# Performance work log

Hardware: AMD Instinct MI355X
Metric: run time of the kernel (lower is better)

Reference implementation:

```python
import jax, jax.numpy as jnp
import numpy as np

DIST_EPS = 0.1   # distance_eps
NORM_EPS = 0.1   # norm_eps
QUAT_EPS = 1e-3
FA_EPS = 1e-5


def normed_vec(V):
    return V / jnp.sqrt((V ** 2).sum(-1, keepdims=True) + NORM_EPS)


def collect_neighbors(node_h, edge_idx):
    # node_h: (B,N,D), edge_idx: (B,N,K) -> (B,N,K,D)
    B, N, K = edge_idx.shape
    D = node_h.shape[-1]
    idx = jnp.broadcast_to(edge_idx.reshape(B, N * K, 1), (B, N * K, D))
    return jnp.take_along_axis(node_h, idx, axis=1).reshape(B, N, K, D)


def field_average(node_h, C, num_fields):
    # per-field mean, scattered back to residues; residues with C==0 get 0
    onehot = (C[..., None] == (jnp.arange(num_fields) + 1)).astype(node_h.dtype)  # (B,N,F)
    sums = jnp.einsum('bnf,bnd->bfd', onehot, node_h)
    counts = jnp.sum(onehot, axis=1)[..., None]  # (B,F,1)
    avg = sums / (counts + FA_EPS)
    return jnp.einsum('bnf,bfd->bnd', onehot, avg)


def reference_frames(X):
    X_N, X_CA, X_C = X[:, :, 0], X[:, :, 1], X[:, :, 2]
    u_CA_N = normed_vec(X_N - X_CA)
    u_CA_C = normed_vec(X_C - X_CA)
    n_1 = u_CA_N
    n_2 = normed_vec(jnp.cross(n_1, u_CA_C))
    n_3 = normed_vec(jnp.cross(n_1, n_2))
    return jnp.stack([n_1, n_2, n_3], -1)  # (B,N,3,3), frames as columns


def reference_frames_field(X, C, num_fields):
    X_N, X_CA, X_C = X[:, :, 0], X[:, :, 1], X[:, :, 2]
    u_CA_N_avg = field_average(normed_vec(X_N - X_CA), C, num_fields)
    u_CA_C_avg = field_average(normed_vec(X_C - X_CA), C, num_fields)
    n_1 = normed_vec(u_CA_N_avg)
    n_2 = normed_vec(jnp.cross(n_1, normed_vec(u_CA_C_avg)))
    n_3 = normed_vec(jnp.cross(n_1, n_2))
    return jnp.stack([n_1, n_2, n_3], -1)


def quaternions_from_rotations(R):
    Rf = R.reshape(R.shape[:-2] + (9,))
    R00, R01, R02, R10, R11, R12, R20, R21, R22 = [Rf[..., i] for i in range(9)]
    mag = 0.5 * jnp.sqrt(jnp.abs(1.0 + jnp.stack([
        R00 + R11 + R22,
        R00 - R11 - R22,
        -R00 + R11 - R22,
        -R00 - R11 + R22], -1)) + QUAT_EPS)
    signs = jnp.sign(jnp.stack([
        jnp.ones_like(R00), R21 - R12, R02 - R20, R10 - R01], -1))
    q = signs * mag
    return q / jnp.sqrt((q ** 2).sum(-1, keepdims=True))


def transformation_features(X_i, X_j, R_i, R_j):
    dX = X_j - X_i[:, :, None]                    # (B,N,K,3)
    L = jnp.sqrt((dX ** 2).sum(-1, keepdims=True) + DIST_EPS)
    u_ij = jnp.einsum('niab,nija->nijb', R_i, dX / L)
    R_rel = jnp.einsum('niab,nijac->nijbc', R_i, R_j)
    q_ij = quaternions_from_rotations(R_rel)
    return jnp.concatenate([jnp.log(L + DIST_EPS), u_ij, q_ij], -1)  # (B,N,K,8)


def setup_inputs() -> dict:
    key = jax.random.key(0)
    k1, k2, k3 = jax.random.split(key, 3)
    B, N, K, NF = 4, 8192, 48, 16
    X = jax.random.normal(k1, (B, N, 4, 3), dtype=jnp.float32)
    edge_idx = jax.random.randint(k2, (B, N, K), 0, N).astype(jnp.int64)
    C = jax.random.randint(k3, (B, N), 0, NF + 1).astype(jnp.int64)
    return {"X": X, "edge_idx": edge_idx, "C": C, "num_fields": NF}


def reference(X, edge_idx, C, num_fields):
    B, N = X.shape[:2]
    R_i = reference_frames(X)
    R_field_i = reference_frames_field(X, C, num_fields)
    X_i = X[:, :, 1, :]  # CA
    X_j = collect_neighbors(X_i, edge_idx)
    X_field_i = field_average(X_i, C, num_fields)
    X_field_j = collect_neighbors(X_field_i, edge_idx)
    R_field_j = collect_neighbors(R_field_i.reshape(B, N, 9), edge_idx).reshape(B, N, -1, 3, 3)
    R_j = collect_neighbors(R_i.reshape(B, N, 9), edge_idx).reshape(B, N, -1, 3, 3)
    h_ff = transformation_features(X_field_i, X_field_j, R_field_i, R_field_j)
    h_fn = transformation_features(X_field_i, X_j, R_field_i, R_j)
    h_nn = transformation_features(X_i, X_j, R_i, R_j)
    edge_h = jnp.concatenate([h_ff, h_fn, h_nn], -1)  # (B,N,K,24)
    mask_i = (C > 0).astype(edge_h.dtype)[..., None]  # (B,N,1)
    mask_j = collect_neighbors(mask_i, edge_idx)      # (B,N,K,1)
    mask_ij = mask_i[:, :, None] * mask_j
    return mask_ij * edge_h
```

## Files before the change

### kernel.cpp

```cpp
#include <hip/hip_runtime.h>
#include <math.h>

#define NFIELDS 16
#define BATCH   4
#define R64_STRIDE 10

#define DIST_EPS 0.1
#define NORM_EPS 0.1
#define QUAT_EPS 0.001
#define FA_EPS   1e-5

#define TAU_NN 2e-5f
#define TAU_FN 2e-6f

typedef float f32x4 __attribute__((ext_vector_type(4)));

#define FS_THREADS 256
__global__ void prep_pass(const float* __restrict__ X, const int* __restrict__ C,
                          double* __restrict__ Rws64, float* __restrict__ nodeF2,
                          double* __restrict__ accum,
                          int N, int BN, int nodeBlocks) {
    __shared__ double red[FS_THREADS][10];
    int t = threadIdx.x;

    if ((int)blockIdx.x < nodeBlocks) {
        int bn = blockIdx.x * blockDim.x + t;
        if (bn >= BN) return;
        const float* xp = X + (size_t)bn * 12;
        double ax = xp[3], ay = xp[4], az = xp[5];

        double ux = (double)xp[0] - ax, uy = (double)xp[1] - ay, uz = (double)xp[2] - az;
        double r1 = 1.0 / sqrt(ux * ux + uy * uy + uz * uz + NORM_EPS);
        ux *= r1; uy *= r1; uz *= r1;

        double vx = (double)xp[6] - ax, vy = (double)xp[7] - ay, vz = (double)xp[8] - az;
        double r2 = 1.0 / sqrt(vx * vx + vy * vy + vz * vz + NORM_EPS);
        vx *= r2; vy *= r2; vz *= r2;

        double wx = uy * vz - uz * vy, wy = uz * vx - ux * vz, wz = ux * vy - uy * vx;
        double r3 = 1.0 / sqrt(wx * wx + wy * wy + wz * wz + NORM_EPS);
        wx *= r3; wy *= r3; wz *= r3;

        double px = uy * wz - uz * wy, py = uz * wx - ux * wz, pz = ux * wy - uy * wx;
        double r4 = 1.0 / sqrt(px * px + py * py + pz * pz + NORM_EPS);
        px *= r4; py *= r4; pz *= r4;

        double* R = Rws64 + (size_t)bn * R64_STRIDE;
        R[0] = ux; R[1] = uy; R[2] = uz;
        R[3] = wx; R[4] = wy; R[5] = wz;
        R[6] = px; R[7] = py; R[8] = pz;

        int c = C[bn];
        float4* nf = (float4*)(nodeF2 + (size_t)bn * 16);
        nf[0] = make_float4((float)ux, (float)uy, (float)uz, (float)wx);
        nf[1] = make_float4((float)wy, (float)wz, xp[3], xp[4]);
        nf[2] = make_float4(xp[5], (float)c, (float)px, (float)py);
        nf[3] = make_float4((float)pz, 0.f, 0.f, 0.f);
        return;
    }

    int fb = blockIdx.x - nodeBlocks;
    int b  = fb / NFIELDS;
    int f  = fb % NFIELDS + 1;
    const float* Xb = X + (size_t)b * N * 12;
    const int*   Cb = C + (size_t)b * N;

    double s[10];
#pragma unroll
    for (int i = 0; i < 10; i++) s[i] = 0.0;

    for (int n = t; n < N; n += FS_THREADS) {
        if (Cb[n] == f) {
            const float* xp = Xb + (size_t)n * 12;
            double ax = xp[3], ay = xp[4], az = xp[5];
            double ux = (double)xp[0] - ax, uy = (double)xp[1] - ay, uz = (double)xp[2] - az;
            double r1 = 1.0 / sqrt(ux * ux + uy * uy + uz * uz + NORM_EPS);
            double vx = (double)xp[6] - ax, vy = (double)xp[7] - ay, vz = (double)xp[8] - az;
            double r2 = 1.0 / sqrt(vx * vx + vy * vy + vz * vz + NORM_EPS);
            s[0] += ux * r1; s[1] += uy * r1; s[2] += uz * r1;
            s[3] += vx * r2; s[4] += vy * r2; s[5] += vz * r2;
            s[6] += ax;      s[7] += ay;      s[8] += az;
            s[9] += 1.0;
        }
    }

#pragma unroll
    for (int i = 0; i < 10; i++) red[t][i] = s[i];
    __syncthreads();
    for (int off = FS_THREADS / 2; off > 0; off >>= 1) {
        if (t < off) {
#pragma unroll
            for (int i = 0; i < 10; i++) red[t][i] += red[t + off][i];
        }
        __syncthreads();
    }
    if (t < 10) accum[(size_t)fb * 10 + t] = red[0][t];
}

__device__ __forceinline__ double sgn64(double x) {
    return x > 0.0 ? 1.0 : (x < 0.0 ? -1.0 : 0.0);
}

__device__ __forceinline__ void tf64(double xix, double xiy, double xiz,
                                     double xjx, double xjy, double xjz,
                                     const double* __restrict__ Ri,
                                     const double* __restrict__ Rj,
                                     float* __restrict__ o) {
    double dx = xjx - xix, dy = xjy - xiy, dz = xjz - xiz;
    double L = sqrt(dx * dx + dy * dy + dz * dz + DIST_EPS);
    o[0] = (float)log(L + DIST_EPS);
    double il = 1.0 / L;
    double vx = dx * il, vy = dy * il, vz = dz * il;
    o[1] = (float)(Ri[0] * vx + Ri[1] * vy + Ri[2] * vz);
    o[2] = (float)(Ri[3] * vx + Ri[4] * vy + Ri[5] * vz);
    o[3] = (float)(Ri[6] * vx + Ri[7] * vy + Ri[8] * vz);

    double r00 = Ri[0] * Rj[0] + Ri[1] * Rj[1] + Ri[2] * Rj[2];
    double r01 = Ri[0] * Rj[3] + Ri[1] * Rj[4] + Ri[2] * Rj[5];
    double r02 = Ri[0] * Rj[6] + Ri[1] * Rj[7] + Ri[2] * Rj[8];
    double r10 = Ri[3] * Rj[0] + Ri[4] * Rj[1] + Ri[5] * Rj[2];
    double r11 = Ri[3] * Rj[3] + Ri[4] * Rj[4] + Ri[5] * Rj[5];
    double r12 = Ri[3] * Rj[6] + Ri[4] * Rj[7] + Ri[5] * Rj[8];
    double r20 = Ri[6] * Rj[0] + Ri[7] * Rj[1] + Ri[8] * Rj[2];
    double r21 = Ri[6] * Rj[3] + Ri[7] * Rj[4] + Ri[8] * Rj[5];
    double r22 = Ri[6] * Rj[6] + Ri[7] * Rj[7] + Ri[8] * Rj[8];

    double m0 = 0.5 * sqrt(fabs(1.0 + r00 + r11 + r22) + QUAT_EPS);
    double m1 = 0.5 * sqrt(fabs(1.0 + r00 - r11 - r22) + QUAT_EPS);
    double m2 = 0.5 * sqrt(fabs(1.0 - r00 + r11 - r22) + QUAT_EPS);
    double m3 = 0.5 * sqrt(fabs(1.0 - r00 - r11 + r22) + QUAT_EPS);
    double q0 = m0;
    double q1 = sgn64(r21 - r12) * m1;
    double q2 = sgn64(r02 - r20) * m2;
    double q3 = sgn64(r10 - r01) * m3;
    double qn = 1.0 / sqrt(q0 * q0 + q1 * q1 + q2 * q2 + q3 * q3);
    o[4] = (float)(q0 * qn); o[5] = (float)(q1 * qn);
    o[6] = (float)(q2 * qn); o[7] = (float)(q3 * qn);
}

__global__ void field_finish(const double* __restrict__ accum,
                             double* __restrict__ table64,
                             float* __restrict__ tableF,
                             float* __restrict__ hff) {
    int b = blockIdx.x;
    int t = threadIdx.x;

    if (t <= NFIELDS) {
        double* e = table64 + ((size_t)b * (NFIELDS + 1) + t) * 12;
        float*  eF = tableF + ((size_t)b * (NFIELDS + 1) + t) * 12;
        if (t == 0) {
#pragma unroll
            for (int i = 0; i < 12; i++) { e[i] = 0.0; eF[i] = 0.f; }
        } else {
            const double* s = accum + (size_t)(b * NFIELDS + t - 1) * 10;
            double inv = 1.0 / (s[9] + FA_EPS);
            double axv = s[0] * inv, ayv = s[1] * inv, azv = s[2] * inv;
            double bxv = s[3] * inv, byv = s[4] * inv, bzv = s[5] * inv;
            double xx  = s[6] * inv, xy  = s[7] * inv, xz  = s[8] * inv;

            double r1 = 1.0 / sqrt(axv * axv + ayv * ayv + azv * azv + NORM_EPS);
            double n1x = axv * r1, n1y = ayv * r1, n1z = azv * r1;
            double r2 = 1.0 / sqrt(bxv * bxv + byv * byv + bzv * bzv + NORM_EPS);
            bxv *= r2; byv *= r2; bzv *= r2;

            double wx = n1y * bzv - n1z * byv, wy = n1z * bxv - n1x * bzv, wz = n1x * byv - n1y * bxv;
            double r3 = 1.0 / sqrt(wx * wx + wy * wy + wz * wz + NORM_EPS);
            wx *= r3; wy *= r3; wz *= r3;

            double px = n1y * wz - n1z * wy, py = n1z * wx - n1x * wz, pz = n1x * wy - n1y * wx;
            double r4 = 1.0 / sqrt(px * px + py * py + pz * pz + NORM_EPS);
            px *= r4; py *= r4; pz *= r4;

            e[0] = n1x; e[1] = n1y; e[2] = n1z;
            e[3] = wx;  e[4] = wy;  e[5] = wz;
            e[6] = px;  e[7] = py;  e[8] = pz;
            e[9] = xx;  e[10] = xy; e[11] = xz;
#pragma unroll
            for (int i = 0; i < 12; i++) eF[i] = (float)e[i];
        }
    }
    __syncthreads();

    int ci = t >> 4, cj = t & 15;
    const double* fi = table64 + ((size_t)b * (NFIELDS + 1) + ci + 1) * 12;
    const double* fj = table64 + ((size_t)b * (NFIELDS + 1) + cj + 1) * 12;
    float o[8];
    tf64(fi[9], fi[10], fi[11], fj[9], fj[10], fj[11], fi, fj, o);
    float* hp = hff + (((size_t)b * NFIELDS + ci) * NFIELDS + cj) * 8;
    ((float4*)hp)[0] = make_float4(o[0], o[1], o[2], o[3]);
    ((float4*)hp)[1] = make_float4(o[4], o[5], o[6], o[7]);
}

__device__ __forceinline__ void tf32(float xix, float xiy, float xiz,
                                     float xjx, float xjy, float xjz,
                                     const float* __restrict__ Ri,
                                     const float* __restrict__ Rj,
                                     float s1, float s2, float s3,
                                     float* __restrict__ o) {
    float dx = xjx - xix, dy = xjy - xiy, dz = xjz - xiz;
    float d2 = dx * dx + dy * dy + dz * dz + 0.1f;
    float ril = rsqrtf(d2);
    float L = d2 * ril;
    o[0] = __logf(L + 0.1f);
    float vx = dx * ril, vy = dy * ril, vz = dz * ril;
    o[1] = Ri[0] * vx + Ri[1] * vy + Ri[2] * vz;
    o[2] = Ri[3] * vx + Ri[4] * vy + Ri[5] * vz;
    o[3] = Ri[6] * vx + Ri[7] * vy + Ri[8] * vz;

    float r00 = Ri[0] * Rj[0] + Ri[1] * Rj[1] + Ri[2] * Rj[2];
    float r11 = Ri[3] * Rj[3] + Ri[4] * Rj[4] + Ri[5] * Rj[5];
    float r22 = Ri[6] * Rj[6] + Ri[7] * Rj[7] + Ri[8] * Rj[8];

    float y0 = fabsf(1.f + r00 + r11 + r22) + 0.001f;
    float y1 = fabsf(1.f + r00 - r11 - r22) + 0.001f;
    float y2 = fabsf(1.f - r00 + r11 - r22) + 0.001f;
    float y3 = fabsf(1.f - r00 - r11 + r22) + 0.001f;
    float q0 = 0.5f * y0 * rsqrtf(y0);
    float q1 = s1 * (0.5f * y1 * rsqrtf(y1));
    float q2 = s2 * (0.5f * y2 * rsqrtf(y2));
    float q3 = s3 * (0.5f * y3 * rsqrtf(y3));
    float qn = rsqrtf(q0 * q0 + q1 * q1 + q2 * q2 + q3 * q3);
    o[4] = q0 * qn; o[5] = q1 * qn; o[6] = q2 * qn; o[7] = q3 * qn;
}

__device__ __forceinline__ float fsgnd(double x) {
    return x > 0.0 ? 1.f : (x < 0.0 ? -1.f : 0.f);
}
__device__ __forceinline__ int hswz(int idx16) {
    return idx16 ^ ((idx16 >> 3) & 7);
}
__device__ __forceinline__ void n3_recompute(const float* __restrict__ r ,
                                             float* __restrict__ n3) {
    float px = r[1] * r[5] - r[2] * r[4];
    float py = r[2] * r[3] - r[0] * r[5];
    float pz = r[0] * r[4] - r[1] * r[3];
    float rr = rsqrtf(px * px + py * py + pz * pz + 0.1f);
    n3[0] = px * rr; n3[1] = py * rr; n3[2] = pz * rr;
}

__device__ __forceinline__ void edge_core(
        const float* __restrict__ rj, const float* __restrict__ cjp,
        const float* __restrict__ ri, const float* __restrict__ cip,
        const float* __restrict__ fF, const float* __restrict__ fp,
        const double* __restrict__ Rws64, const double* __restrict__ table64,
        int b, int bn, int bj, int cn, float* __restrict__ o) {
    float a21 = ri[6]*rj[3] + ri[7]*rj[4] + ri[8]*rj[5] - (ri[3]*rj[6] + ri[4]*rj[7] + ri[5]*rj[8]);
    float a02 = ri[0]*rj[6] + ri[1]*rj[7] + ri[2]*rj[8] - (ri[6]*rj[0] + ri[7]*rj[1] + ri[8]*rj[2]);
    float a10 = ri[3]*rj[0] + ri[4]*rj[1] + ri[5]*rj[2] - (ri[0]*rj[3] + ri[1]*rj[4] + ri[2]*rj[5]);
    float g21 = fF[6]*rj[3] + fF[7]*rj[4] + fF[8]*rj[5] - (fF[3]*rj[6] + fF[4]*rj[7] + fF[5]*rj[8]);
    float g02 = fF[0]*rj[6] + fF[1]*rj[7] + fF[2]*rj[8] - (fF[6]*rj[0] + fF[7]*rj[1] + fF[8]*rj[2]);
    float g10 = fF[3]*rj[0] + fF[4]*rj[1] + fF[5]*rj[2] - (fF[0]*rj[3] + fF[1]*rj[4] + fF[2]*rj[5]);

    float sa21 = copysignf(1.f, a21), sa02 = copysignf(1.f, a02), sa10 = copysignf(1.f, a10);
    float sg21 = copysignf(1.f, g21), sg02 = copysignf(1.f, g02), sg10 = copysignf(1.f, g10);

    float amin = fminf(fminf(fabsf(a21), fabsf(a02)), fabsf(a10));
    float gmin = fminf(fminf(fabsf(g21), fabsf(g02)), fabsf(g10));
    if (amin < TAU_NN || gmin < TAU_FN) {
        const double* RJ = Rws64 + (size_t)bj * R64_STRIDE;
        const double* RI = Rws64 + (size_t)bn * R64_STRIDE;
        const double* FD = table64 + ((size_t)b * (NFIELDS + 1) + cn) * 12;
        double d21 = RI[6]*RJ[3] + RI[7]*RJ[4] + RI[8]*RJ[5] - (RI[3]*RJ[6] + RI[4]*RJ[7] + RI[5]*RJ[8]);
        double d02 = RI[0]*RJ[6] + RI[1]*RJ[7] + RI[2]*RJ[8] - (RI[6]*RJ[0] + RI[7]*RJ[1] + RI[8]*RJ[2]);
        double d10 = RI[3]*RJ[0] + RI[4]*RJ[1] + RI[5]*RJ[2] - (RI[0]*RJ[3] + RI[1]*RJ[4] + RI[2]*RJ[5]);
        double e21 = FD[6]*RJ[3] + FD[7]*RJ[4] + FD[8]*RJ[5] - (FD[3]*RJ[6] + FD[4]*RJ[7] + FD[5]*RJ[8]);
        double e02 = FD[0]*RJ[6] + FD[1]*RJ[7] + FD[2]*RJ[8] - (FD[6]*RJ[0] + FD[7]*RJ[1] + FD[8]*RJ[2]);
        double e10 = FD[3]*RJ[0] + FD[4]*RJ[1] + FD[5]*RJ[2] - (FD[0]*RJ[3] + FD[1]*RJ[4] + FD[2]*RJ[5]);
        sa21 = fsgnd(d21); sa02 = fsgnd(d02); sa10 = fsgnd(d10);
        sg21 = fsgnd(e21); sg02 = fsgnd(e02); sg10 = fsgnd(e10);
    }

    tf32(fp[0], fp[1], fp[2], cjp[0], cjp[1], cjp[2], fF, rj, sg21, sg02, sg10, o + 8);
    tf32(cip[0], cip[1], cip[2], cjp[0], cjp[1], cjp[2], ri, rj, sa21, sa02, sa10, o + 16);
}

template <int KC, int NC>
__global__ __launch_bounds__(256)
void edge_pass_lds(const float* __restrict__ nodeF2, const int* __restrict__ eidx,
                   const float* __restrict__ tableF, const float* __restrict__ hff,
                   const double* __restrict__ Rws64, const double* __restrict__ table64,
                   float* __restrict__ out) {
    __shared__ float4 s_hff[2 * NFIELDS * NFIELDS];
    __shared__ float4 s_tf[(NFIELDS + 1) * 3];
    __shared__ float  s_st[256 * 28];

    const int t   = threadIdx.x;
    const int b   = blockIdx.x / ((KC * NC) / 256);
    const int tid = blockIdx.x * 256 + t;
    const int bn  = tid / KC;
    const int bj  = b * NC + eidx[tid];

    const float4* rjp = (const float4*)(nodeF2 + (size_t)bj * 16);
    float4 j0 = rjp[0], j1 = rjp[1], j2 = rjp[2];
    const float4* rip = (const float4*)(nodeF2 + (size_t)bn * 16);
    float4 i0 = rip[0], i1 = rip[1], i2 = rip[2], i3 = rip[3];

    {
        const float4* src = (const float4*)(hff + (size_t)b * (NFIELDS * NFIELDS * 8));
        s_hff[hswz(t)]       = src[t];
        s_hff[hswz(t + 256)] = src[t + 256];
        if (t < (NFIELDS + 1) * 3)
            s_tf[t] = ((const float4*)(tableF + (size_t)b * (NFIELDS + 1) * 12))[t];
    }
    __syncthreads();

    const int cj = (int)j2.y;
    const int cn = (int)i2.y;
    const bool valid = (cn > 0) && (cj > 0);

    float o[24];
    if (valid) {
        float rj[9] = { j0.x, j0.y, j0.z, j0.w, j1.x, j1.y, 0, 0, 0 };
        float cjp[3] = { j1.z, j1.w, j2.x };
        n3_recompute(rj, rj + 6);
        float ri[9] = { i0.x, i0.y, i0.z, i0.w, i1.x, i1.y, i2.z, i2.w, i3.x };
        float cip[3] = { i1.z, i1.w, i2.x };

        float fF[9], fp[3];
        float4 f0 = s_tf[cn * 3 + 0], f1 = s_tf[cn * 3 + 1], f2 = s_tf[cn * 3 + 2];
        fF[0] = f0.x; fF[1] = f0.y; fF[2] = f0.z; fF[3] = f0.w;
        fF[4] = f1.x; fF[5] = f1.y; fF[6] = f1.z; fF[7] = f1.w;
        fF[8] = f2.x; fp[0] = f2.y; fp[1] = f2.z; fp[2] = f2.w;

        edge_core(rj, cjp, ri, cip, fF, fp, Rws64, table64, b, bn, bj, cn, o);

        int e = ((cn - 1) * NFIELDS + (cj - 1)) * 2;
        float4 h0 = s_hff[hswz(e)];
        float4 h1 = s_hff[hswz(e + 1)];
        o[0] = h0.x; o[1] = h0.y; o[2] = h0.z; o[3] = h0.w;
        o[4] = h1.x; o[5] = h1.y; o[6] = h1.z; o[7] = h1.w;
    } else {
#pragma unroll
        for (int i = 0; i < 24; i++) o[i] = 0.f;
    }

#pragma unroll
    for (int c = 0; c < 6; c++)
        *(float4*)(s_st + t * 28 + c * 4) =
            make_float4(o[4*c], o[4*c+1], o[4*c+2], o[4*c+3]);
    __syncthreads();

    f32x4* outv = (f32x4*)out + (size_t)blockIdx.x * 1536;
#pragma unroll
    for (int r = 0; r < 6; r++) {
        int f  = t + 256 * r;
        int el = f / 6, c = f - el * 6;
        f32x4 v = *(const f32x4*)(s_st + el * 28 + c * 4);
        __builtin_nontemporal_store(v, outv + f);
    }
}

__global__ void edge_pass_gen(const float* __restrict__ nodeF2,
                              const int* __restrict__ eidx,
                              const float* __restrict__ tableF,
                              const float* __restrict__ hff,
                              const double* __restrict__ Rws64,
                              const double* __restrict__ table64,
                              float* __restrict__ out,
                              int N, int K, int total) {
    int tid = blockIdx.x * blockDim.x + threadIdx.x;
    if (tid >= total) return;
    int bn = tid / K;
    int b  = bn / N;
    int bj = b * N + eidx[tid];

    const float4* rjp = (const float4*)(nodeF2 + (size_t)bj * 16);
    float4 j0 = rjp[0], j1 = rjp[1], j2 = rjp[2], j3 = rjp[3];
    const float4* rip = (const float4*)(nodeF2 + (size_t)bn * 16);
    float4 i0 = rip[0], i1 = rip[1], i2 = rip[2], i3 = rip[3];
    int cj = (int)j2.y;
    int cn = (int)i2.y;

    float o[24];
    if (cn > 0 && cj > 0) {
        float rj[9] = { j0.x, j0.y, j0.z, j0.w, j1.x, j1.y, j2.z, j2.w, j3.x };
        float cjp[3] = { j1.z, j1.w, j2.x };
        float ri[9] = { i0.x, i0.y, i0.z, i0.w, i1.x, i1.y, i2.z, i2.w, i3.x };
        float cip[3] = { i1.z, i1.w, i2.x };

        const float4* ftp = (const float4*)(tableF + ((size_t)b * (NFIELDS + 1) + cn) * 12);
        float4 f0 = ftp[0], f1 = ftp[1], f2 = ftp[2];
        float fF[9] = { f0.x, f0.y, f0.z, f0.w, f1.x, f1.y, f1.z, f1.w, f2.x };
        float fp[3] = { f2.y, f2.z, f2.w };

        const float4* hp = (const float4*)(hff +
            (((size_t)b * NFIELDS + (cn - 1)) * NFIELDS + (cj - 1)) * 8);
        float4 h0 = hp[0], h1 = hp[1];
        o[0] = h0.x; o[1] = h0.y; o[2] = h0.z; o[3] = h0.w;
        o[4] = h1.x; o[5] = h1.y; o[6] = h1.z; o[7] = h1.w;
        edge_core(rj, cjp, ri, cip, fF, fp, Rws64, table64, b, bn, bj, cn, o);
    } else {
#pragma unroll
        for (int i = 0; i < 24; i++) o[i] = 0.f;
    }

    float4* op = (float4*)(out + (size_t)tid * 24);
#pragma unroll
    for (int i = 0; i < 6; i++)
        op[i] = make_float4(o[4 * i], o[4 * i + 1], o[4 * i + 2], o[4 * i + 3]);
}

extern "C" void kernel_launch(void* const* d_in, const int* in_sizes, int n_in,
                              void* d_out, int out_size, void* d_ws, size_t ws_size,
                              hipStream_t stream) {
    const float* X  = (const float*)d_in[0];
    const int* eidx = (const int*)d_in[1];
    const int* C    = (const int*)d_in[2];

    const int B  = BATCH;
    const int BN = in_sizes[2];
    const int N  = BN / B;
    const int total = in_sizes[1];
    const int K  = total / BN;

    double* accum   = (double*)d_ws;
    double* table64 = accum + B * NFIELDS * 10;
    double* Rws64   = table64 + B * (NFIELDS + 1) * 12;
    float*  nodeF2  = (float*)(Rws64 + (size_t)BN * R64_STRIDE);
    float*  tableF  = nodeF2 + (size_t)BN * 16;
    float*  hff     = tableF + B * (NFIELDS + 1) * 12;

    int nodeBlocks = (BN + 255) / 256;
    prep_pass<<<nodeBlocks + B * NFIELDS, FS_THREADS, 0, stream>>>(
        X, C, Rws64, nodeF2, accum, N, BN, nodeBlocks);
    field_finish<<<B, 256, 0, stream>>>(accum, table64, tableF, hff);

    if (K == 48 && N == 8192 && (total % 256) == 0) {
        edge_pass_lds<48, 8192><<<total / 256, 256, 0, stream>>>(
            nodeF2, eidx, tableF, hff, Rws64, table64, (float*)d_out);
    } else {
        int eb = (total + 255) / 256;
        edge_pass_gen<<<eb, 256, 0, stream>>>(nodeF2, eidx, tableF, hff,
                                              Rws64, table64, (float*)d_out,
                                              N, K, total);
    }
}
```

Measured before the change: 63.83 us.

## Precompute field-to-neighbor features per (field, node) pair in a separate pass

The h_fn features depend only on the source residue's field and the neighbor node, so a new kernel computes them once for every (batch, field, node) combination, using exact double-precision signs, and writes them to workspace. The edge kernel then gathers these 8 floats per edge instead of recomputing the field-frame transform and its sign fallback. This removes per-edge arithmetic and divergent double-precision branches, at the cost of an extra kernel launch, a B*16*N*8-float workspace table, and an extra random gather per edge. The path is taken only when the workspace is large enough.

```diff
diff --git a/kernel.cpp b/kernel.cpp
--- a/kernel.cpp
+++ b/kernel.cpp
@@ -238,57 +238,58 @@
     n3[0] = px * rr; n3[1] = py * rr; n3[2] = pz * rr;
 }
 
-__device__ __forceinline__ void edge_core(
-        const float* __restrict__ rj, const float* __restrict__ cjp,
-        const float* __restrict__ ri, const float* __restrict__ cip,
-        const float* __restrict__ fF, const float* __restrict__ fp,
-        const double* __restrict__ Rws64, const double* __restrict__ table64,
-        int b, int bn, int bj, int cn, float* __restrict__ o) {
-    float a21 = ri[6]*rj[3] + ri[7]*rj[4] + ri[8]*rj[5] - (ri[3]*rj[6] + ri[4]*rj[7] + ri[5]*rj[8]);
-    float a02 = ri[0]*rj[6] + ri[1]*rj[7] + ri[2]*rj[8] - (ri[6]*rj[0] + ri[7]*rj[1] + ri[8]*rj[2]);
-    float a10 = ri[3]*rj[0] + ri[4]*rj[1] + ri[5]*rj[2] - (ri[0]*rj[3] + ri[1]*rj[4] + ri[2]*rj[5]);
-    float g21 = fF[6]*rj[3] + fF[7]*rj[4] + fF[8]*rj[5] - (fF[3]*rj[6] + fF[4]*rj[7] + fF[5]*rj[8]);
-    float g02 = fF[0]*rj[6] + fF[1]*rj[7] + fF[2]*rj[8] - (fF[6]*rj[0] + fF[7]*rj[1] + fF[8]*rj[2]);
-    float g10 = fF[3]*rj[0] + fF[4]*rj[1] + fF[5]*rj[2] - (fF[0]*rj[3] + fF[1]*rj[4] + fF[2]*rj[5]);
-
-    float sa21 = copysignf(1.f, a21), sa02 = copysignf(1.f, a02), sa10 = copysignf(1.f, a10);
-    float sg21 = copysignf(1.f, g21), sg02 = copysignf(1.f, g02), sg10 = copysignf(1.f, g10);
-
-    float amin = fminf(fminf(fabsf(a21), fabsf(a02)), fabsf(a10));
-    float gmin = fminf(fminf(fabsf(g21), fabsf(g02)), fabsf(g10));
-    if (amin < TAU_NN || gmin < TAU_FN) {
-        const double* RJ = Rws64 + (size_t)bj * R64_STRIDE;
-        const double* RI = Rws64 + (size_t)bn * R64_STRIDE;
-        const double* FD = table64 + ((size_t)b * (NFIELDS + 1) + cn) * 12;
-        double d21 = RI[6]*RJ[3] + RI[7]*RJ[4] + RI[8]*RJ[5] - (RI[3]*RJ[6] + RI[4]*RJ[7] + RI[5]*RJ[8]);
-        double d02 = RI[0]*RJ[6] + RI[1]*RJ[7] + RI[2]*RJ[8] - (RI[6]*RJ[0] + RI[7]*RJ[1] + RI[8]*RJ[2]);
-        double d10 = RI[3]*RJ[0] + RI[4]*RJ[1] + RI[5]*RJ[2] - (RI[0]*RJ[3] + RI[1]*RJ[4] + RI[2]*RJ[5]);
-        double e21 = FD[6]*RJ[3] + FD[7]*RJ[4] + FD[8]*RJ[5] - (FD[3]*RJ[6] + FD[4]*RJ[7] + FD[5]*RJ[8]);
-        double e02 = FD[0]*RJ[6] + FD[1]*RJ[7] + FD[2]*RJ[8] - (FD[6]*RJ[0] + FD[7]*RJ[1] + FD[8]*RJ[2]);
-        double e10 = FD[3]*RJ[0] + FD[4]*RJ[1] + FD[5]*RJ[2] - (FD[0]*RJ[3] + FD[1]*RJ[4] + FD[2]*RJ[5]);
-        sa21 = fsgnd(d21); sa02 = fsgnd(d02); sa10 = fsgnd(d10);
-        sg21 = fsgnd(e21); sg02 = fsgnd(e02); sg10 = fsgnd(e10);
-    }
-
-    tf32(fp[0], fp[1], fp[2], cjp[0], cjp[1], cjp[2], fF, rj, sg21, sg02, sg10, o + 8);
-    tf32(cip[0], cip[1], cip[2], cjp[0], cjp[1], cjp[2], ri, rj, sa21, sa02, sa10, o + 16);
+template <int NC>
+__global__ __launch_bounds__(256)
+void hfn_pass(const float* __restrict__ nodeF2, const float* __restrict__ tableF,
+              const double* __restrict__ table64, const double* __restrict__ Rws64,
+              float* __restrict__ hfn) {
+    int idx = blockIdx.x * 256 + threadIdx.x;
+    int j   = idx & (NC - 1);
+    int bf  = idx / NC;
+    int b   = bf >> 4;
+    int fi  = bf & 15;
+    int bn  = b * NC + j;
+
+    const float4* rjp = (const float4*)(nodeF2 + (size_t)bn * 16);
+    float4 j0 = rjp[0], j1 = rjp[1], j2 = rjp[2];
+    float rj[9] = { j0.x, j0.y, j0.z, j0.w, j1.x, j1.y, 0, 0, 0 };
+    float cjp[3] = { j1.z, j1.w, j2.x };
+    n3_recompute(rj, rj + 6);
+
+    const float4* ftp = (const float4*)(tableF + ((size_t)b * (NFIELDS + 1) + fi + 1) * 12);
+    float4 f0 = ftp[0], f1 = ftp[1], f2 = ftp[2];
+    float fF[9] = { f0.x, f0.y, f0.z, f0.w, f1.x, f1.y, f1.z, f1.w, f2.x };
+    float fp[3] = { f2.y, f2.z, f2.w };
+
+    const double* RJ = Rws64 + (size_t)bn * R64_STRIDE;
+    const double* FD = table64 + ((size_t)b * (NFIELDS + 1) + fi + 1) * 12;
+    double e21 = FD[6]*RJ[3] + FD[7]*RJ[4] + FD[8]*RJ[5] - (FD[3]*RJ[6] + FD[4]*RJ[7] + FD[5]*RJ[8]);
+    double e02 = FD[0]*RJ[6] + FD[1]*RJ[7] + FD[2]*RJ[8] - (FD[6]*RJ[0] + FD[7]*RJ[1] + FD[8]*RJ[2]);
+    double e10 = FD[3]*RJ[0] + FD[4]*RJ[1] + FD[5]*RJ[2] - (FD[0]*RJ[3] + FD[1]*RJ[4] + FD[2]*RJ[5]);
+
+    float o[8];
+    tf32(fp[0], fp[1], fp[2], cjp[0], cjp[1], cjp[2], fF, rj,
+         fsgnd(e21), fsgnd(e02), fsgnd(e10), o);
+
+    float4* hp = (float4*)(hfn + (size_t)idx * 8);
+    hp[0] = make_float4(o[0], o[1], o[2], o[3]);
+    hp[1] = make_float4(o[4], o[5], o[6], o[7]);
 }
 
 template <int KC, int NC>
 __global__ __launch_bounds__(256)
 void edge_pass_lds(const float* __restrict__ nodeF2, const int* __restrict__ eidx,
-                   const float* __restrict__ tableF, const float* __restrict__ hff,
-                   const double* __restrict__ Rws64, const double* __restrict__ table64,
-                   float* __restrict__ out) {
+                   const float* __restrict__ hfn, const float* __restrict__ hff,
+                   const double* __restrict__ Rws64, float* __restrict__ out) {
     __shared__ float4 s_hff[2 * NFIELDS * NFIELDS];
-    __shared__ float4 s_tf[(NFIELDS + 1) * 3];
     __shared__ float  s_st[256 * 28];
 
     const int t   = threadIdx.x;
     const int b   = blockIdx.x / ((KC * NC) / 256);
     const int tid = blockIdx.x * 256 + t;
     const int bn  = tid / KC;
-    const int bj  = b * NC + eidx[tid];
+    const int j   = eidx[tid];
+    const int bj  = b * NC + j;
 
     const float4* rjp = (const float4*)(nodeF2 + (size_t)bj * 16);
     float4 j0 = rjp[0], j1 = rjp[1], j2 = rjp[2];
@@ -299,8 +300,6 @@
         const float4* src = (const float4*)(hff + (size_t)b * (NFIELDS * NFIELDS * 8));
         s_hff[hswz(t)]       = src[t];
         s_hff[hswz(t + 256)] = src[t + 256];
-        if (t < (NFIELDS + 1) * 3)
-            s_tf[t] = ((const float4*)(tableF + (size_t)b * (NFIELDS + 1) * 12))[t];
     }
     __syncthreads();
 
@@ -310,19 +309,33 @@
 
     float o[24];
     if (valid) {
+        const float4* hf = (const float4*)(hfn +
+            (((size_t)(b * NFIELDS + (cn - 1)) * NC) + j) * 8);
+        float4 hn0 = hf[0], hn1 = hf[1];
+        o[8]  = hn0.x; o[9]  = hn0.y; o[10] = hn0.z; o[11] = hn0.w;
+        o[12] = hn1.x; o[13] = hn1.y; o[14] = hn1.z; o[15] = hn1.w;
+
         float rj[9] = { j0.x, j0.y, j0.z, j0.w, j1.x, j1.y, 0, 0, 0 };
-        float cjp[3] = { j1.z, j1.w, j2.x };
+        float cjpv[3] = { j1.z, j1.w, j2.x };
         n3_recompute(rj, rj + 6);
         float ri[9] = { i0.x, i0.y, i0.z, i0.w, i1.x, i1.y, i2.z, i2.w, i3.x };
-        float cip[3] = { i1.z, i1.w, i2.x };
-
-        float fF[9], fp[3];
-        float4 f0 = s_tf[cn * 3 + 0], f1 = s_tf[cn * 3 + 1], f2 = s_tf[cn * 3 + 2];
-        fF[0] = f0.x; fF[1] = f0.y; fF[2] = f0.z; fF[3] = f0.w;
-        fF[4] = f1.x; fF[5] = f1.y; fF[6] = f1.z; fF[7] = f1.w;
-        fF[8] = f2.x; fp[0] = f2.y; fp[1] = f2.z; fp[2] = f2.w;
-
-        edge_core(rj, cjp, ri, cip, fF, fp, Rws64, table64, b, bn, bj, cn, o);
+        float cipv[3] = { i1.z, i1.w, i2.x };
+
+        float a21 = ri[6]*rj[3] + ri[7]*rj[4] + ri[8]*rj[5] - (ri[3]*rj[6] + ri[4]*rj[7] + ri[5]*rj[8]);
+        float a02 = ri[0]*rj[6] + ri[1]*rj[7] + ri[2]*rj[8] - (ri[6]*rj[0] + ri[7]*rj[1] + ri[8]*rj[2]);
+        float a10 = ri[3]*rj[0] + ri[4]*rj[1] + ri[5]*rj[2] - (ri[0]*rj[3] + ri[1]*rj[4] + ri[2]*rj[5]);
+        float sa21 = copysignf(1.f, a21), sa02 = copysignf(1.f, a02), sa10 = copysignf(1.f, a10);
+        float amin = fminf(fminf(fabsf(a21), fabsf(a02)), fabsf(a10));
+        if (amin < TAU_NN) {
+            const double* RJ = Rws64 + (size_t)bj * R64_STRIDE;
+            const double* RI = Rws64 + (size_t)bn * R64_STRIDE;
+            double d21 = RI[6]*RJ[3] + RI[7]*RJ[4] + RI[8]*RJ[5] - (RI[3]*RJ[6] + RI[4]*RJ[7] + RI[5]*RJ[8]);
+            double d02 = RI[0]*RJ[6] + RI[1]*RJ[7] + RI[2]*RJ[8] - (RI[6]*RJ[0] + RI[7]*RJ[1] + RI[8]*RJ[2]);
+            double d10 = RI[3]*RJ[0] + RI[4]*RJ[1] + RI[5]*RJ[2] - (RI[0]*RJ[3] + RI[1]*RJ[4] + RI[2]*RJ[5]);
+            sa21 = fsgnd(d21); sa02 = fsgnd(d02); sa10 = fsgnd(d10);
+        }
+        tf32(cipv[0], cipv[1], cipv[2], cjpv[0], cjpv[1], cjpv[2],
+             ri, rj, sa21, sa02, sa10, o + 16);
 
         int e = ((cn - 1) * NFIELDS + (cj - 1)) * 2;
         float4 h0 = s_hff[hswz(e)];
@@ -374,9 +387,9 @@
     float o[24];
     if (cn > 0 && cj > 0) {
         float rj[9] = { j0.x, j0.y, j0.z, j0.w, j1.x, j1.y, j2.z, j2.w, j3.x };
-        float cjp[3] = { j1.z, j1.w, j2.x };
+        float cjpv[3] = { j1.z, j1.w, j2.x };
         float ri[9] = { i0.x, i0.y, i0.z, i0.w, i1.x, i1.y, i2.z, i2.w, i3.x };
-        float cip[3] = { i1.z, i1.w, i2.x };
+        float cipv[3] = { i1.z, i1.w, i2.x };
 
         const float4* ftp = (const float4*)(tableF + ((size_t)b * (NFIELDS + 1) + cn) * 12);
         float4 f0 = ftp[0], f1 = ftp[1], f2 = ftp[2];
@@ -388,7 +401,32 @@
         float4 h0 = hp[0], h1 = hp[1];
         o[0] = h0.x; o[1] = h0.y; o[2] = h0.z; o[3] = h0.w;
         o[4] = h1.x; o[5] = h1.y; o[6] = h1.z; o[7] = h1.w;
-        edge_core(rj, cjp, ri, cip, fF, fp, Rws64, table64, b, bn, bj, cn, o);
+
+        float a21 = ri[6]*rj[3] + ri[7]*rj[4] + ri[8]*rj[5] - (ri[3]*rj[6] + ri[4]*rj[7] + ri[5]*rj[8]);
+        float a02 = ri[0]*rj[6] + ri[1]*rj[7] + ri[2]*rj[8] - (ri[6]*rj[0] + ri[7]*rj[1] + ri[8]*rj[2]);
+        float a10 = ri[3]*rj[0] + ri[4]*rj[1] + ri[5]*rj[2] - (ri[0]*rj[3] + ri[1]*rj[4] + ri[2]*rj[5]);
+        float g21 = fF[6]*rj[3] + fF[7]*rj[4] + fF[8]*rj[5] - (fF[3]*rj[6] + fF[4]*rj[7] + fF[5]*rj[8]);
+        float g02 = fF[0]*rj[6] + fF[1]*rj[7] + fF[2]*rj[8] - (fF[6]*rj[0] + fF[7]*rj[1] + fF[8]*rj[2]);
+        float g10 = fF[3]*rj[0] + fF[4]*rj[1] + fF[5]*rj[2] - (fF[0]*rj[3] + fF[1]*rj[4] + fF[2]*rj[5]);
+        float sa21 = copysignf(1.f, a21), sa02 = copysignf(1.f, a02), sa10 = copysignf(1.f, a10);
+        float sg21 = copysignf(1.f, g21), sg02 = copysignf(1.f, g02), sg10 = copysignf(1.f, g10);
+        float amin = fminf(fminf(fabsf(a21), fabsf(a02)), fabsf(a10));
+        float gmin = fminf(fminf(fabsf(g21), fabsf(g02)), fabsf(g10));
+        if (amin < TAU_NN || gmin < TAU_FN) {
+            const double* RJ = Rws64 + (size_t)bj * R64_STRIDE;
+            const double* RI = Rws64 + (size_t)bn * R64_STRIDE;
+            const double* FD = table64 + ((size_t)b * (NFIELDS + 1) + cn) * 12;
+            double d21 = RI[6]*RJ[3] + RI[7]*RJ[4] + RI[8]*RJ[5] - (RI[3]*RJ[6] + RI[4]*RJ[7] + RI[5]*RJ[8]);
+            double d02 = RI[0]*RJ[6] + RI[1]*RJ[7] + RI[2]*RJ[8] - (RI[6]*RJ[0] + RI[7]*RJ[1] + RI[8]*RJ[2]);
+            double d10 = RI[3]*RJ[0] + RI[4]*RJ[1] + RI[5]*RJ[2] - (RI[0]*RJ[3] + RI[1]*RJ[4] + RI[2]*RJ[5]);
+            double e21 = FD[6]*RJ[3] + FD[7]*RJ[4] + FD[8]*RJ[5] - (FD[3]*RJ[6] + FD[4]*RJ[7] + FD[5]*RJ[8]);
+            double e02 = FD[0]*RJ[6] + FD[1]*RJ[7] + FD[2]*RJ[8] - (FD[6]*RJ[0] + FD[7]*RJ[1] + FD[8]*RJ[2]);
+            double e10 = FD[3]*RJ[0] + FD[4]*RJ[1] + FD[5]*RJ[2] - (FD[0]*RJ[3] + FD[1]*RJ[4] + FD[2]*RJ[5]);
+            sa21 = fsgnd(d21); sa02 = fsgnd(d02); sa10 = fsgnd(d10);
+            sg21 = fsgnd(e21); sg02 = fsgnd(e02); sg10 = fsgnd(e10);
+        }
+        tf32(fp[0], fp[1], fp[2], cjpv[0], cjpv[1], cjpv[2], fF, rj, sg21, sg02, sg10, o + 8);
+        tf32(cipv[0], cipv[1], cipv[2], cjpv[0], cjpv[1], cjpv[2], ri, rj, sa21, sa02, sa10, o + 16);
     } else {
 #pragma unroll
         for (int i = 0; i < 24; i++) o[i] = 0.f;
@@ -419,15 +457,20 @@
     float*  nodeF2  = (float*)(Rws64 + (size_t)BN * R64_STRIDE);
     float*  tableF  = nodeF2 + (size_t)BN * 16;
     float*  hff     = tableF + B * (NFIELDS + 1) * 12;
+    float*  hfn     = hff + B * NFIELDS * NFIELDS * 8;
+
+    size_t need_bytes = (size_t)((char*)(hfn + (size_t)B * NFIELDS * N * 8) - (char*)d_ws);
 
     int nodeBlocks = (BN + 255) / 256;
     prep_pass<<<nodeBlocks + B * NFIELDS, FS_THREADS, 0, stream>>>(
         X, C, Rws64, nodeF2, accum, N, BN, nodeBlocks);
     field_finish<<<B, 256, 0, stream>>>(accum, table64, tableF, hff);
 
-    if (K == 48 && N == 8192 && (total % 256) == 0) {
+    if (K == 48 && N == 8192 && (total % 256) == 0 && ws_size >= need_bytes) {
+        hfn_pass<8192><<<(B * NFIELDS * N) / 256, 256, 0, stream>>>(
+            nodeF2, tableF, table64, Rws64, hfn);
         edge_pass_lds<48, 8192><<<total / 256, 256, 0, stream>>>(
-            nodeF2, eidx, tableF, hff, Rws64, table64, (float*)d_out);
+            nodeF2, eidx, hfn, hff, Rws64, (float*)d_out);
     } else {
         int eb = (total + 255) / 256;
         edge_pass_gen<<<eb, 256, 0, stream>>>(nodeF2, eidx, tableF, hff,
```

After: 89.60 us. +40.4%, slower.

## Drop LDS table staging and halve output staging buffer to raise occupancy

Applied to the files above, without the earlier changes.

The edge kernel no longer copies the per-batch hff and field-frame tables into shared memory. It reads them directly from global memory per edge, which removes one block barrier and the LDS swizzle. The output staging buffer is halved, and the transposed coalesced store now runs in two rounds of 128 threads each. The goal is lower LDS use per block so more blocks fit on each CU. In exchange each edge issues extra global or L2 gathers, and the store phase adds two more barriers.

```diff
diff --git a/kernel.cpp b/kernel.cpp
--- a/kernel.cpp
+++ b/kernel.cpp
@@ -226,9 +226,6 @@
 __device__ __forceinline__ float fsgnd(double x) {
     return x > 0.0 ? 1.f : (x < 0.0 ? -1.f : 0.f);
 }
-__device__ __forceinline__ int hswz(int idx16) {
-    return idx16 ^ ((idx16 >> 3) & 7);
-}
 __device__ __forceinline__ void n3_recompute(const float* __restrict__ r ,
                                              float* __restrict__ n3) {
     float px = r[1] * r[5] - r[2] * r[4];
@@ -280,9 +277,7 @@
                    const float* __restrict__ tableF, const float* __restrict__ hff,
                    const double* __restrict__ Rws64, const double* __restrict__ table64,
                    float* __restrict__ out) {
-    __shared__ float4 s_hff[2 * NFIELDS * NFIELDS];
-    __shared__ float4 s_tf[(NFIELDS + 1) * 3];
-    __shared__ float  s_st[256 * 28];
+    __shared__ float s_st[128 * 28];
 
     const int t   = threadIdx.x;
     const int b   = blockIdx.x / ((KC * NC) / 256);
@@ -295,15 +290,6 @@
     const float4* rip = (const float4*)(nodeF2 + (size_t)bn * 16);
     float4 i0 = rip[0], i1 = rip[1], i2 = rip[2], i3 = rip[3];
 
-    {
-        const float4* src = (const float4*)(hff + (size_t)b * (NFIELDS * NFIELDS * 8));
-        s_hff[hswz(t)]       = src[t];
-        s_hff[hswz(t + 256)] = src[t + 256];
-        if (t < (NFIELDS + 1) * 3)
-            s_tf[t] = ((const float4*)(tableF + (size_t)b * (NFIELDS + 1) * 12))[t];
-    }
-    __syncthreads();
-
     const int cj = (int)j2.y;
     const int cn = (int)i2.y;
     const bool valid = (cn > 0) && (cj > 0);
@@ -311,40 +297,57 @@
     float o[24];
     if (valid) {
         float rj[9] = { j0.x, j0.y, j0.z, j0.w, j1.x, j1.y, 0, 0, 0 };
-        float cjp[3] = { j1.z, j1.w, j2.x };
+        float cjpv[3] = { j1.z, j1.w, j2.x };
         n3_recompute(rj, rj + 6);
         float ri[9] = { i0.x, i0.y, i0.z, i0.w, i1.x, i1.y, i2.z, i2.w, i3.x };
-        float cip[3] = { i1.z, i1.w, i2.x };
-
-        float fF[9], fp[3];
-        float4 f0 = s_tf[cn * 3 + 0], f1 = s_tf[cn * 3 + 1], f2 = s_tf[cn * 3 + 2];
-        fF[0] = f0.x; fF[1] = f0.y; fF[2] = f0.z; fF[3] = f0.w;
-        fF[4] = f1.x; fF[5] = f1.y; fF[6] = f1.z; fF[7] = f1.w;
-        fF[8] = f2.x; fp[0] = f2.y; fp[1] = f2.z; fp[2] = f2.w;
-
-        edge_core(rj, cjp, ri, cip, fF, fp, Rws64, table64, b, bn, bj, cn, o);
-
-        int e = ((cn - 1) * NFIELDS + (cj - 1)) * 2;
-        float4 h0 = s_hff[hswz(e)];
-        float4 h1 = s_hff[hswz(e + 1)];
+        float cipv[3] = { i1.z, i1.w, i2.x };
+
+        const float4* ftp = (const float4*)(tableF + ((size_t)b * (NFIELDS + 1) + cn) * 12);
+        float4 f0 = ftp[0], f1 = ftp[1], f2 = ftp[2];
+        float fF[9] = { f0.x, f0.y, f0.z, f0.w, f1.x, f1.y, f1.z, f1.w, f2.x };
+        float fp[3] = { f2.y, f2.z, f2.w };
+
+        const float4* hp = (const float4*)(hff +
+            (((size_t)b * NFIELDS + (cn - 1)) * NFIELDS + (cj - 1)) * 8);
+        float4 h0 = hp[0], h1 = hp[1];
         o[0] = h0.x; o[1] = h0.y; o[2] = h0.z; o[3] = h0.w;
         o[4] = h1.x; o[5] = h1.y; o[6] = h1.z; o[7] = h1.w;
+
+        edge_core(rj, cjpv, ri, cipv, fF, fp, Rws64, table64, b, bn, bj, cn, o);
     } else {
 #pragma unroll
         for (int i = 0; i < 24; i++) o[i] = 0.f;
     }
 
-#pragma unroll
-    for (int c = 0; c < 6; c++)
-        *(float4*)(s_st + t * 28 + c * 4) =
-            make_float4(o[4*c], o[4*c+1], o[4*c+2], o[4*c+3]);
+    f32x4* outv = (f32x4*)out + (size_t)blockIdx.x * 1536;
+
+    if (t < 128) {
+#pragma unroll
+        for (int c = 0; c < 6; c++)
+            *(float4*)(s_st + t * 28 + c * 4) =
+                make_float4(o[4*c], o[4*c+1], o[4*c+2], o[4*c+3]);
+    }
     __syncthreads();
-
-    f32x4* outv = (f32x4*)out + (size_t)blockIdx.x * 1536;
-#pragma unroll
-    for (int r = 0; r < 6; r++) {
+#pragma unroll
+    for (int r = 0; r < 3; r++) {
         int f  = t + 256 * r;
         int el = f / 6, c = f - el * 6;
+        f32x4 v = *(const f32x4*)(s_st + el * 28 + c * 4);
+        __builtin_nontemporal_store(v, outv + f);
+    }
+    __syncthreads();
+    if (t >= 128) {
+#pragma unroll
+        for (int c = 0; c < 6; c++)
+            *(float4*)(s_st + (t - 128) * 28 + c * 4) =
+                make_float4(o[4*c], o[4*c+1], o[4*c+2], o[4*c+3]);
+    }
+    __syncthreads();
+#pragma unroll
+    for (int r = 0; r < 3; r++) {
+        int f  = 768 + t + 256 * r;
+        int fe = f / 6;
+        int el = fe - 128, c = f - fe * 6;
         f32x4 v = *(const f32x4*)(s_st + el * 28 + c * 4);
         __builtin_nontemporal_store(v, outv + f);
     }
@@ -374,9 +377,9 @@
     float o[24];
     if (cn > 0 && cj > 0) {
         float rj[9] = { j0.x, j0.y, j0.z, j0.w, j1.x, j1.y, j2.z, j2.w, j3.x };
-        float cjp[3] = { j1.z, j1.w, j2.x };
+        float cjpv[3] = { j1.z, j1.w, j2.x };
         float ri[9] = { i0.x, i0.y, i0.z, i0.w, i1.x, i1.y, i2.z, i2.w, i3.x };
-        float cip[3] = { i1.z, i1.w, i2.x };
+        float cipv[3] = { i1.z, i1.w, i2.x };
 
         const float4* ftp = (const float4*)(tableF + ((size_t)b * (NFIELDS + 1) + cn) * 12);
         float4 f0 = ftp[0], f1 = ftp[1], f2 = ftp[2];
@@ -388,7 +391,7 @@
         float4 h0 = hp[0], h1 = hp[1];
         o[0] = h0.x; o[1] = h0.y; o[2] = h0.z; o[3] = h0.w;
         o[4] = h1.x; o[5] = h1.y; o[6] = h1.z; o[7] = h1.w;
-        edge_core(rj, cjp, ri, cip, fF, fp, Rws64, table64, b, bn, bj, cn, o);
+        edge_core(rj, cjpv, ri, cipv, fF, fp, Rws64, table64, b, bn, bj, cn, o);
     } else {
 #pragma unroll
         for (int i = 0; i < 24; i++) o[i] = 0.f;
```

Measured after the change: 63.99 us. About the same (+0.3%).
